# Optimization experiments

Measured on AMD Instinct MI355X. Metric: run time of the kernel, lower is better.

The kernel has to match this reference:

```python
import jax, jax.numpy as jnp
import numpy as np

EPS = 1e-5
NUM_HEADS = 8
BLOCK_SIZE = 8


def _ln(x, w, b):
    mu = jnp.mean(x, axis=-1, keepdims=True)
    var = jnp.mean((x - mu) ** 2, axis=-1, keepdims=True)
    return (x - mu) * jax.lax.rsqrt(var + EPS) * w + b


def _mha(x, wqkv, bqkv, wo, bo, allowed):
    # x: [b,t,d]; wqkv: [3d,d]; allowed: [t,t] bool (True = attend)
    b, t, d = x.shape
    h, hd = NUM_HEADS, d // NUM_HEADS
    qkv = x @ wqkv.T + bqkv
    q, k, v = jnp.split(qkv, 3, axis=-1)
    q = q.reshape(b, t, h, hd)
    k = k.reshape(b, t, h, hd)
    v = v.reshape(b, t, h, hd)
    scores = jnp.einsum('bihd,bjhd->bhij', q, k) / np.sqrt(hd).astype(x.dtype)
    scores = jnp.where(allowed[None, None], scores, -jnp.inf)
    attn = jax.nn.softmax(scores, axis=-1)
    out = jnp.einsum('bhij,bjhd->bihd', attn, v).reshape(b, t, d)
    return out @ wo.T + bo


def setup_inputs() -> dict:
    key = jax.random.key(0)
    ks = jax.random.split(key, 20)
    B, T, D, FF, L, MAXT = 64, 512, 256, 512, 4, 512
    s = 0.02
    return {
        'latents': jax.random.normal(ks[0], (B, T, D), dtype=jnp.float32),
        'move_ids': jax.random.randint(ks[1], (B, T), 0, 20480),
        'mask': jax.random.randint(ks[2], (B, T), 0, 2).astype(bool),
        'positional': s * jax.random.normal(ks[3], (1, MAXT, D), dtype=jnp.float32),
        'embed_from': s * jax.random.normal(ks[4], (64, D), dtype=jnp.float32),
        'embed_to': s * jax.random.normal(ks[5], (64, D), dtype=jnp.float32),
        'embed_promo': s * jax.random.normal(ks[6], (5, D), dtype=jnp.float32),
        'in_proj_w': s * jax.random.normal(ks[7], (L, 3 * D, D), dtype=jnp.float32),
        'in_proj_b': jnp.zeros((L, 3 * D), dtype=jnp.float32),
        'out_w': s * jax.random.normal(ks[8], (L, D, D), dtype=jnp.float32),
        'out_b': jnp.zeros((L, D), dtype=jnp.float32),
        'fc1_w': s * jax.random.normal(ks[9], (L, FF, D), dtype=jnp.float32),
        'fc1_b': jnp.zeros((L, FF), dtype=jnp.float32),
        'fc2_w': s * jax.random.normal(ks[10], (L, D, FF), dtype=jnp.float32),
        'fc2_b': jnp.zeros((L, D), dtype=jnp.float32),
        'norm_w': jnp.ones((D,), dtype=jnp.float32),
        'norm_b': jnp.zeros((D,), dtype=jnp.float32),
    }


def reference(latents, move_ids, mask, positional, embed_from, embed_to,
              embed_promo, in_proj_w, in_proj_b, out_w, out_b,
              fc1_w, fc1_b, fc2_w, fc2_b, norm_w, norm_b):
    b, t, d = latents.shape
    # move-id decomposition: promo/from/to embedding sum
    promo = move_ids // 4096
    rem = move_ids % 4096
    frm = rem // 64
    to = rem % 64
    x = latents + positional[:, :t, :] + embed_from[frm] + embed_to[to] + embed_promo[promo]
    # block-causal mask: token i may attend j iff block(j) <= block(i)
    bidx = jnp.arange(t) // BLOCK_SIZE
    allowed = bidx[None, :] <= bidx[:, None]
    n_layers = in_proj_w.shape[0]
    for l in range(n_layers):
        # NOTE: the single LayerNorm (norm_w, norm_b) is shared everywhere,
        # exactly as in the original module.
        x = x + _mha(_ln(x, norm_w, norm_b), in_proj_w[l], in_proj_b[l],
                     out_w[l], out_b[l], allowed)
        h1 = jax.nn.relu(_ln(x, norm_w, norm_b) @ fc1_w[l].T + fc1_b[l])
        x = x + h1 @ fc2_w[l].T + fc2_b[l]
    x = _ln(x, norm_w, norm_b)
    return jnp.where(mask[..., None], x, latents)
```

## Files before the change

### kernel.cpp

```cpp
#include <hip/hip_runtime.h>
#include <math.h>

#define Bv  64
#define Tv  512
#define Dv  256
#define FFv 512
#define Lv  4
#define BTv (Bv*Tv)
#define EPSv 1e-5f
#define QSC 0.25509402f

typedef __attribute__((ext_vector_type(8))) short short8;
typedef __attribute__((ext_vector_type(4))) float f32x4;
typedef unsigned short us;

#if __has_builtin(__builtin_amdgcn_exp2f)
#define EXP2(x) __builtin_amdgcn_exp2f(x)
#else
#define EXP2(x) exp2f(x)
#endif

__device__ __forceinline__ us f2bf(float f) {
    unsigned r;
    asm("v_cvt_pk_bf16_f32 %0, %1, 0" : "=v"(r) : "v"(f));
    return (us)r;
}
__device__ __forceinline__ unsigned pk2(float a, float b) {
    unsigned r;
    asm("v_cvt_pk_bf16_f32 %0, %1, %2" : "=v"(r) : "v"(a), "v"(b));
    return r;
}
__device__ __forceinline__ float wave_sum(float v) {
#pragma unroll
    for (int o = 32; o > 0; o >>= 1) v += __shfl_xor(v, o);
    return v;
}

__global__ __launch_bounds__(256) void cvtall_kernel(
    const float* __restrict__ qw, const float* __restrict__ ow,
    const float* __restrict__ f1, const float* __restrict__ f2,
    const float* __restrict__ qb,
    us* __restrict__ wq, us* __restrict__ wo, us* __restrict__ w1,
    us* __restrict__ w2, float* __restrict__ sb)
{
    int blk = blockIdx.x, tid = threadIdx.x;
    if (blk < 2048) {
        const float* s; us* d; int i; float sc = 1.0f;
        if (blk < 768)       { i = blk*256 + tid;        s = qw; d = wq;
                               sc = (((i >> 6) % 768) < 256) ? QSC : 1.0f; }
        else if (blk < 1024) { i = (blk-768)*256 + tid;  s = ow; d = wo; }
        else if (blk < 1536) { i = (blk-1024)*256 + tid; s = f1; d = w1; }
        else                 { i = (blk-1536)*256 + tid; s = f2; d = w2; }
        float4 v = ((const float4*)s)[i];
        uint2 o;
        o.x = pk2(v.x*sc, v.y*sc);
        o.y = pk2(v.z*sc, v.w*sc);
        ((uint2*)d)[i] = o;
    } else {
        int i = (blk-2048)*256 + tid;
        sb[i] = qb[i] * (((i % 768) < 256) ? QSC : 1.0f);
    }
}

__global__ __launch_bounds__(256) void embed_ln_kernel(
    const float* __restrict__ lat, const int* __restrict__ mids,
    const float* __restrict__ pos, const float* __restrict__ ef,
    const float* __restrict__ et,  const float* __restrict__ ep,
    const float* __restrict__ nw,  const float* __restrict__ nb,
    float* __restrict__ x, us* __restrict__ xn)
{
    int wv = threadIdx.x >> 6, lane = threadIdx.x & 63;
    size_t row = (size_t)blockIdx.x * 4 + wv;
    int t  = (int)(row & (Tv - 1));
    int id = mids[row];
    int promo = id >> 12;
    int rem   = id & 4095;
    int frm   = rem >> 6;
    int to    = rem & 63;
    float4 v  = ((const float4*)(lat + row*Dv))[lane];
    float4 pv = ((const float4*)(pos + (size_t)t*Dv))[lane];
    float4 fv = ((const float4*)(ef + (size_t)frm*Dv))[lane];
    float4 tv = ((const float4*)(et + (size_t)to*Dv))[lane];
    float4 ev = ((const float4*)(ep + (size_t)promo*Dv))[lane];
    v.x += pv.x + fv.x + tv.x + ev.x;
    v.y += pv.y + fv.y + tv.y + ev.y;
    v.z += pv.z + fv.z + tv.z + ev.z;
    v.w += pv.w + fv.w + tv.w + ev.w;
    ((float4*)(x + row*Dv))[lane] = v;
    float mu = wave_sum(v.x + v.y + v.z + v.w) * (1.0f/Dv);
    float dx = v.x-mu, dy = v.y-mu, dz = v.z-mu, dw = v.w-mu;
    float var = wave_sum(dx*dx + dy*dy + dz*dz + dw*dw) * (1.0f/Dv);
    float inv = rsqrtf(var + EPSv);
    float4 w4 = ((const float4*)nw)[lane];
    float4 b4 = ((const float4*)nb)[lane];
    uint2 o;
    o.x = pk2(dx*inv*w4.x + b4.x, dy*inv*w4.y + b4.y);
    o.y = pk2(dz*inv*w4.z + b4.z, dw*inv*w4.w + b4.w);
    ((uint2*)(xn + row*Dv))[lane] = o;
}

__global__ __launch_bounds__(256) void final_kernel(
    const float* __restrict__ x, const float* __restrict__ lat,
    const int* __restrict__ mask, const float* __restrict__ w,
    const float* __restrict__ b, float* __restrict__ out)
{
    int wv = threadIdx.x >> 6, lane = threadIdx.x & 63;
    size_t row = (size_t)blockIdx.x * 4 + wv;
    float4 v = ((const float4*)(x + row*Dv))[lane];
    float mu = wave_sum(v.x + v.y + v.z + v.w) * (1.0f/Dv);
    float dx = v.x-mu, dy = v.y-mu, dz = v.z-mu, dw = v.w-mu;
    float var = wave_sum(dx*dx + dy*dy + dz*dz + dw*dw) * (1.0f/Dv);
    float inv = rsqrtf(var + EPSv);
    float4 w4 = ((const float4*)w)[lane];
    float4 b4 = ((const float4*)b)[lane];
    float4 o;
    o.x = dx*inv*w4.x + b4.x;
    o.y = dy*inv*w4.y + b4.y;
    o.z = dz*inv*w4.z + b4.z;
    o.w = dw*inv*w4.w + b4.w;
    if (!mask[row]) o = ((const float4*)(lat + row*Dv))[lane];
    ((float4*)(out + row*Dv))[lane] = o;
}

template<int RELU>
__global__ __launch_bounds__(512, 2) void mm256sq_kernel(
    const us* __restrict__ A, const us* __restrict__ B,
    const float* __restrict__ bias, us* __restrict__ C,
    int M, int N, int K)
{
    __shared__ us As[2][256*64];
    __shared__ us Bs[2][256*64];
    int tid  = threadIdx.x;
    int lane = tid & 63;
    int wu   = __builtin_amdgcn_readfirstlane(tid >> 6);
    int m0 = blockIdx.x * 256, n0 = blockIdx.y * 256;
    int wm = wu & 1, wn = wu >> 1;
    f32x4 acc[8][4] = {};
    int srow = lane >> 3;
    int sg   = (lane & 7) ^ srow;
    const us* Ag = A + (size_t)m0 * K + sg*8;
    const us* Bg = B + (size_t)n0 * K + sg*8;
    int cc = lane & 15, q4 = lane >> 4;

#define STG(kk, bb) { \
    _Pragma("unroll") \
    for (int p = 0; p < 4; p++) { \
        int row = wu*32 + p*8; \
        __builtin_amdgcn_global_load_lds( \
            (const __attribute__((address_space(1))) unsigned int*)(Ag + (size_t)(row + srow)*K + (kk)), \
            (__attribute__((address_space(3))) unsigned int*)(&As[bb][row*64]), \
            16, 0, 0); \
        __builtin_amdgcn_global_load_lds( \
            (const __attribute__((address_space(1))) unsigned int*)(Bg + (size_t)(row + srow)*K + (kk)), \
            (__attribute__((address_space(3))) unsigned int*)(&Bs[bb][row*64]), \
            16, 0, 0); \
    } }

    STG(0, 0);
    __syncthreads();
    int nk = K >> 6;
    int cur = 0;
    for (int t = 0; t < nk; t++) {
        if (t + 1 < nk) {
            if (cur) STG((t+1)*64, 0) else STG((t+1)*64, 1)
        }
#pragma unroll
        for (int h = 0; h < 2; h++) {
            int pg = ((h*4 + q4) ^ (cc & 7)) * 8;
            short8 av[8], bv[4];
#pragma unroll
            for (int i = 0; i < 8; i++)
                av[i] = *(const short8*)(&As[cur][(wm*128 + i*16 + cc)*64 + pg]);
#pragma unroll
            for (int j = 0; j < 4; j++)
                bv[j] = *(const short8*)(&Bs[cur][(wn*64 + j*16 + cc)*64 + pg]);
#pragma unroll
            for (int i = 0; i < 8; i++)
#pragma unroll
                for (int j = 0; j < 4; j++)
                    acc[i][j] = __builtin_amdgcn_mfma_f32_16x16x32_bf16(av[i], bv[j], acc[i][j], 0, 0, 0);
        }
        __syncthreads();
        cur ^= 1;
    }
#undef STG
#pragma unroll
    for (int j = 0; j < 4; j++) {
        int n = n0 + wn*64 + j*16 + cc;
        float bj = bias[n];
#pragma unroll
        for (int i = 0; i < 8; i++) {
#pragma unroll
            for (int r = 0; r < 4; r++) {
                int m = m0 + wm*128 + i*16 + q4*4 + r;
                float v = acc[i][j][r] + bj;
                if (RELU) v = fmaxf(v, 0.f);
                C[(size_t)m * N + n] = f2bf(v);
            }
        }
    }
}

__global__ __launch_bounds__(256) void mm256_kernel(
    const us* __restrict__ A, const us* __restrict__ B,
    const float* __restrict__ bias, float* __restrict__ x,
    us* __restrict__ xn, const float* __restrict__ nw,
    const float* __restrict__ nb, int M, int K)
{
    __shared__ us As[64*64];
    __shared__ us Bs[256*64];
    __shared__ float red[64][4][2];
    __shared__ float mus[64], rss[64];
    int tid  = threadIdx.x;
    int lane = tid & 63;
    int wu   = __builtin_amdgcn_readfirstlane(tid >> 6);
    int m0 = blockIdx.x * 64;
    f32x4 acc[4][4] = {};
    int srow = lane >> 3;
    int sg   = (lane & 7) ^ srow;
    const us* Ag = A + (size_t)m0 * K + sg*8;
    const us* Bg = B + sg*8;
    int cc = lane & 15, q4 = lane >> 4;
    for (int k0 = 0; k0 < K; k0 += 64) {
        __syncthreads();
#pragma unroll
        for (int p = 0; p < 2; p++) {
            int row = wu*16 + p*8;
            __builtin_amdgcn_global_load_lds(
                (const __attribute__((address_space(1))) unsigned int*)(Ag + (size_t)(row + srow)*K + k0),
                (__attribute__((address_space(3))) unsigned int*)(As + row*64),
                16, 0, 0);
        }
#pragma unroll
        for (int p = 0; p < 8; p++) {
            int row = wu*64 + p*8;
            __builtin_amdgcn_global_load_lds(
                (const __attribute__((address_space(1))) unsigned int*)(Bg + (size_t)(row + srow)*K + k0),
                (__attribute__((address_space(3))) unsigned int*)(Bs + row*64),
                16, 0, 0);
        }
        __syncthreads();
#pragma unroll
        for (int h = 0; h < 2; h++) {
            int pg = ((h*4 + q4) ^ (cc & 7)) * 8;
            short8 av[4], bv[4];
#pragma unroll
            for (int i = 0; i < 4; i++)
                av[i] = *(const short8*)(As + (i*16 + cc)*64 + pg);
#pragma unroll
            for (int j = 0; j < 4; j++)
                bv[j] = *(const short8*)(Bs + (wu*64 + j*16 + cc)*64 + pg);
#pragma unroll
            for (int i = 0; i < 4; i++)
#pragma unroll
                for (int j = 0; j < 4; j++)
                    acc[i][j] = __builtin_amdgcn_mfma_f32_16x16x32_bf16(av[i], bv[j], acc[i][j], 0, 0, 0);
        }
    }
    float bb[4], nwv[4], nbv[4];
#pragma unroll
    for (int j = 0; j < 4; j++) {
        int n = wu*64 + j*16 + cc;
        bb[j] = bias[n]; nwv[j] = nw[n]; nbv[j] = nb[n];
    }
#pragma unroll
    for (int i = 0; i < 4; i++) {
        float s[4] = {0.f,0.f,0.f,0.f}, sq[4] = {0.f,0.f,0.f,0.f};
#pragma unroll
        for (int j = 0; j < 4; j++) {
#pragma unroll
            for (int r = 0; r < 4; r++) {
                int m = m0 + i*16 + q4*4 + r;
                size_t off = (size_t)m * Dv + wu*64 + j*16 + cc;
                float v = acc[i][j][r] + bb[j] + x[off];
                acc[i][j][r] = v;
                x[off] = v;
                s[r] += v; sq[r] += v*v;
            }
        }
#pragma unroll
        for (int r = 0; r < 4; r++) {
#pragma unroll
            for (int o = 1; o < 16; o <<= 1) {
                s[r]  += __shfl_xor(s[r],  o);
                sq[r] += __shfl_xor(sq[r], o);
            }
        }
        if (cc == 0) {
#pragma unroll
            for (int r = 0; r < 4; r++) {
                red[i*16 + q4*4 + r][wu][0] = s[r];
                red[i*16 + q4*4 + r][wu][1] = sq[r];
            }
        }
    }
    __syncthreads();
    if (tid < 64) {
        float ts = red[tid][0][0] + red[tid][1][0] + red[tid][2][0] + red[tid][3][0];
        float tq = red[tid][0][1] + red[tid][1][1] + red[tid][2][1] + red[tid][3][1];
        float mu = ts * (1.0f/Dv);
        float var = tq * (1.0f/Dv) - mu*mu;
        mus[tid] = mu;
        rss[tid] = rsqrtf(var + EPSv);
    }
    __syncthreads();
#pragma unroll
    for (int i = 0; i < 4; i++) {
#pragma unroll
        for (int r = 0; r < 4; r++) {
            int ml = i*16 + q4*4 + r;
            float mu = mus[ml], rv = rss[ml];
#pragma unroll
            for (int j = 0; j < 4; j++) {
                size_t off = (size_t)(m0 + ml) * Dv + wu*64 + j*16 + cc;
                xn[off] = f2bf((acc[i][j][r] - mu)*rv*nwv[j] + nbv[j]);
            }
        }
    }
}

__global__ __launch_bounds__(256) void attn_kernel(
    const us* __restrict__ qkv, us* __restrict__ ao)
{
    int blk = blockIdx.x;
    int b  = blk & 63;
    int h  = (blk >> 6) & 7;
    int qt = blk >> 9;
    int i0 = qt << 6;
    int tid = threadIdx.x;
    int lane = tid & 63;
    int wu = tid >> 6;

    __shared__ us Ks[2][64][40];
    __shared__ us Vt[2][32][72];
    __shared__ us Ps[4][16][72];
    __shared__ float Ls[4][16];

    size_t rowbase = (size_t)b * Tv;
    int c = lane & 15, q4 = lane >> 4;

    short8 qfrag = *(const short8*)(qkv + (rowbase + i0 + wu*16 + c)*768 + h*32 + q4*8);

    int skey = tid >> 2, sdc = (tid & 3) << 3;
    int vkey = tid & 63, vg = tid >> 6;
    const us* kgp = qkv + (rowbase + skey)*768 + 256 + h*32 + sdc;
    const us* vgp = qkv + (rowbase + vkey)*768 + 512 + h*32 + vg*8;

    f32x4 oacc[2] = {};
    float lsum = 0.f;
    int ntiles = qt + 1;

    short8 kreg = *(const short8*)(kgp);
    short8 vreg = *(const short8*)(vgp);
    *(short8*)&Ks[0][skey][sdc] = kreg;
#pragma unroll
    for (int j = 0; j < 8; j++) Vt[0][vg*8 + j][vkey] = vreg[j];
    if (ntiles > 1) {
        kreg = *(const short8*)(kgp + 64*768);
        vreg = *(const short8*)(vgp + 64*768);
    }
    __syncthreads();

    for (int kt = 0; kt < ntiles; kt++) {
        int cur = kt & 1;
        if (kt + 1 < ntiles) {
            *(short8*)&Ks[cur^1][skey][sdc] = kreg;
#pragma unroll
            for (int j = 0; j < 8; j++) Vt[cur^1][vg*8 + j][vkey] = vreg[j];
        }
        if (kt + 2 < ntiles) {
            kreg = *(const short8*)(kgp + (size_t)(kt+2)*64*768);
            vreg = *(const short8*)(vgp + (size_t)(kt+2)*64*768);
        }

        f32x4 st[4];
#pragma unroll
        for (int jt = 0; jt < 4; jt++) {
            short8 kf = *(const short8*)&Ks[cur][jt*16 + c][q4*8];
            st[jt] = __builtin_amdgcn_mfma_f32_16x16x32_bf16(kf, qfrag, (f32x4){0.f,0.f,0.f,0.f}, 0, 0, 0);
        }
        bool diag = (kt == ntiles - 1);
#pragma unroll
        for (int jt = 0; jt < 4; jt++) {
            float msk = (!diag || (2*jt + (q4 >> 1) <= 2*wu + (c >> 3))) ? 1.f : 0.f;
            float p0 = EXP2(st[jt][0]) * msk;
            float p1 = EXP2(st[jt][1]) * msk;
            float p2 = EXP2(st[jt][2]) * msk;
            float p3 = EXP2(st[jt][3]) * msk;
            lsum += p0 + p1 + p2 + p3;
            uint2 w2; w2.x = pk2(p0, p1); w2.y = pk2(p2, p3);
            *(uint2*)&Ps[wu][c][jt*16 + q4*4] = w2;
        }
#pragma unroll
        for (int kk = 0; kk < 2; kk++) {
            short8 pf = *(const short8*)&Ps[wu][c][kk*32 + q4*8];
#pragma unroll
            for (int dt = 0; dt < 2; dt++) {
                short8 vf = *(const short8*)&Vt[cur][dt*16 + c][kk*32 + q4*8];
                oacc[dt] = __builtin_amdgcn_mfma_f32_16x16x32_bf16(pf, vf, oacc[dt], 0, 0, 0);
            }
        }
        __syncthreads();
    }

    float l = lsum;
    l += __shfl_xor(l, 16);
    l += __shfl_xor(l, 32);
    if (q4 == 0) Ls[wu][c] = 1.0f / l;
    float4 lv4 = *(const float4*)&Ls[wu][q4*4];
#pragma unroll
    for (int dt = 0; dt < 2; dt++) {
#pragma unroll
        for (int r = 0; r < 4; r++) {
            float li = (r == 0) ? lv4.x : (r == 1) ? lv4.y : (r == 2) ? lv4.z : lv4.w;
            ao[(rowbase + i0 + wu*16 + q4*4 + r)*256 + h*32 + dt*16 + c] = f2bf(oacc[dt][r] * li);
        }
    }
}

extern "C" void kernel_launch(void* const* d_in, const int* in_sizes, int n_in,
                              void* d_out, int out_size, void* d_ws, size_t ws_size,
                              hipStream_t stream)
{
    const float* latents    = (const float*)d_in[0];
    const int*   move_ids   = (const int*)  d_in[1];
    const int*   mask       = (const int*)  d_in[2];
    const float* positional = (const float*)d_in[3];
    const float* embed_from = (const float*)d_in[4];
    const float* embed_to   = (const float*)d_in[5];
    const float* embed_promo= (const float*)d_in[6];
    const float* in_proj_w  = (const float*)d_in[7];
    const float* in_proj_b  = (const float*)d_in[8];
    const float* out_w      = (const float*)d_in[9];
    const float* out_b      = (const float*)d_in[10];
    const float* fc1_w      = (const float*)d_in[11];
    const float* fc1_b      = (const float*)d_in[12];
    const float* fc2_w      = (const float*)d_in[13];
    const float* fc2_b      = (const float*)d_in[14];
    const float* norm_w     = (const float*)d_in[15];
    const float* norm_b     = (const float*)d_in[16];
    float* out = (float*)d_out;

    float* x   = (float*)d_ws;
    float* sb  = x + (size_t)BTv * Dv;
    us* xn  = (us*)(sb + Lv*768);
    us* qkv = xn + (size_t)BTv * Dv;
    us* ao  = qkv + (size_t)BTv * 768;
    us* h1  = ao + (size_t)BTv * Dv;
    us* wq  = h1 + (size_t)BTv * FFv;
    us* wo  = wq + (size_t)Lv * 768 * Dv;
    us* w1  = wo + (size_t)Lv * Dv * Dv;
    us* w2  = w1 + (size_t)Lv * FFv * Dv;

    cvtall_kernel<<<2060, 256, 0, stream>>>(in_proj_w, out_w, fc1_w, fc2_w,
                                            in_proj_b, wq, wo, w1, w2, sb);

    embed_ln_kernel<<<BTv/4, 256, 0, stream>>>(latents, move_ids, positional,
        embed_from, embed_to, embed_promo, norm_w, norm_b, x, xn);

    for (int l = 0; l < Lv; l++) {
        mm256sq_kernel<0><<<dim3(BTv/256, 768/256), 512, 0, stream>>>(
            xn, wq + (size_t)l*768*Dv, sb + l*768, qkv, BTv, 768, Dv);
        attn_kernel<<<Bv*8*(Tv/64), 256, 0, stream>>>(qkv, ao);
        mm256_kernel<<<BTv/64, 256, 0, stream>>>(
            ao, wo + (size_t)l*Dv*Dv, out_b + l*Dv, x, xn, norm_w, norm_b,
            BTv, Dv);
        mm256sq_kernel<1><<<dim3(BTv/256, FFv/256), 512, 0, stream>>>(
            xn, w1 + (size_t)l*FFv*Dv, fc1_b + l*FFv, h1, BTv, FFv, Dv);
        mm256_kernel<<<BTv/64, 256, 0, stream>>>(
            h1, w2 + (size_t)l*Dv*FFv, fc2_b + l*Dv, x, xn, norm_w, norm_b,
            BTv, FFv);
    }
    final_kernel<<<BTv/4, 256, 0, stream>>>(x, latents, mask, norm_w, norm_b, out);
}
```

Baseline: 638.0 us.

## Retile GEMMs: 128x128 single-buffer projections, 128-row double-buffered fused residual-LN GEMM

The QKV and FC1 GEMMs move from 256x256 double-buffered tiles with 512 threads to 128x128 single-buffered tiles with 256 threads. That gives more blocks and lower LDS use per block, at the cost of less data reuse per tile. The fused residual+LayerNorm GEMM moves from 64-row tiles with 4 waves to 128-row tiles with 8 waves (a 2x4 wave grid) and double-buffered LDS staging, with cross-wave row reductions. The aim is better occupancy and load balance for the projections, and better B-matrix reuse plus load/compute overlap for the fused kernel.

```diff
diff --git a/kernel.cpp b/kernel.cpp
--- a/kernel.cpp
+++ b/kernel.cpp
@@ -123,33 +123,107 @@
 }
 
 template<int RELU>
-__global__ __launch_bounds__(512, 2) void mm256sq_kernel(
+__global__ __launch_bounds__(256) void mm_kernel(
     const us* __restrict__ A, const us* __restrict__ B,
     const float* __restrict__ bias, us* __restrict__ C,
     int M, int N, int K)
 {
-    __shared__ us As[2][256*64];
-    __shared__ us Bs[2][256*64];
+    __shared__ us As[128*64];
+    __shared__ us Bs[128*64];
     int tid  = threadIdx.x;
     int lane = tid & 63;
     int wu   = __builtin_amdgcn_readfirstlane(tid >> 6);
-    int m0 = blockIdx.x * 256, n0 = blockIdx.y * 256;
+    int m0 = blockIdx.x * 128, n0 = blockIdx.y * 128;
     int wm = wu & 1, wn = wu >> 1;
-    f32x4 acc[8][4] = {};
+    f32x4 acc[4][4] = {};
     int srow = lane >> 3;
     int sg   = (lane & 7) ^ srow;
     const us* Ag = A + (size_t)m0 * K + sg*8;
     const us* Bg = B + (size_t)n0 * K + sg*8;
     int cc = lane & 15, q4 = lane >> 4;
+    for (int k0 = 0; k0 < K; k0 += 64) {
+        __syncthreads();
+#pragma unroll
+        for (int p = 0; p < 4; p++) {
+            int row = wu*32 + p*8;
+            __builtin_amdgcn_global_load_lds(
+                (const __attribute__((address_space(1))) unsigned int*)(Ag + (size_t)(row + srow)*K + k0),
+                (__attribute__((address_space(3))) unsigned int*)(As + row*64),
+                16, 0, 0);
+            __builtin_amdgcn_global_load_lds(
+                (const __attribute__((address_space(1))) unsigned int*)(Bg + (size_t)(row + srow)*K + k0),
+                (__attribute__((address_space(3))) unsigned int*)(Bs + row*64),
+                16, 0, 0);
+        }
+        __syncthreads();
+#pragma unroll
+        for (int h = 0; h < 2; h++) {
+            int pg = ((h*4 + q4) ^ (cc & 7)) * 8;
+            short8 av[4], bv[4];
+#pragma unroll
+            for (int i = 0; i < 4; i++)
+                av[i] = *(const short8*)(As + (wm*64 + i*16 + cc)*64 + pg);
+#pragma unroll
+            for (int j = 0; j < 4; j++)
+                bv[j] = *(const short8*)(Bs + (wn*64 + j*16 + cc)*64 + pg);
+#pragma unroll
+            for (int i = 0; i < 4; i++)
+#pragma unroll
+                for (int j = 0; j < 4; j++)
+                    acc[i][j] = __builtin_amdgcn_mfma_f32_16x16x32_bf16(av[i], bv[j], acc[i][j], 0, 0, 0);
+        }
+    }
+#pragma unroll
+    for (int j = 0; j < 4; j++) {
+        int n = n0 + wn*64 + j*16 + cc;
+        float bj = bias[n];
+#pragma unroll
+        for (int i = 0; i < 4; i++) {
+#pragma unroll
+            for (int r = 0; r < 4; r++) {
+                int m = m0 + wm*64 + i*16 + q4*4 + r;
+                float v = acc[i][j][r] + bj;
+                if (RELU) v = fmaxf(v, 0.f);
+                C[(size_t)m * N + n] = f2bf(v);
+            }
+        }
+    }
+}
+
+__global__ __launch_bounds__(512) void mmfuse_kernel(
+    const us* __restrict__ A, const us* __restrict__ B,
+    const float* __restrict__ bias, float* __restrict__ x,
+    us* __restrict__ xn, const float* __restrict__ nw,
+    const float* __restrict__ nb, int M, int K)
+{
+    __shared__ us As[2][128*64];
+    __shared__ us Bs[2][256*64];
+    __shared__ float red[128][4][2];
+    __shared__ float mus[128], rss[128];
+    int tid  = threadIdx.x;
+    int lane = tid & 63;
+    int wu   = __builtin_amdgcn_readfirstlane(tid >> 6);
+    int m0 = blockIdx.x * 128;
+    int wm = wu & 1, wn = wu >> 1;
+    f32x4 acc[4][4] = {};
+    int srow = lane >> 3;
+    int sg   = (lane & 7) ^ srow;
+    const us* Ag = A + (size_t)m0 * K + sg*8;
+    const us* Bg = B + sg*8;
+    int cc = lane & 15, q4 = lane >> 4;
 
 #define STG(kk, bb) { \
     _Pragma("unroll") \
-    for (int p = 0; p < 4; p++) { \
-        int row = wu*32 + p*8; \
+    for (int p = 0; p < 2; p++) { \
+        int row = wu*16 + p*8; \
         __builtin_amdgcn_global_load_lds( \
             (const __attribute__((address_space(1))) unsigned int*)(Ag + (size_t)(row + srow)*K + (kk)), \
             (__attribute__((address_space(3))) unsigned int*)(&As[bb][row*64]), \
             16, 0, 0); \
+    } \
+    _Pragma("unroll") \
+    for (int p = 0; p < 4; p++) { \
+        int row = wu*32 + p*8; \
         __builtin_amdgcn_global_load_lds( \
             (const __attribute__((address_space(1))) unsigned int*)(Bg + (size_t)(row + srow)*K + (kk)), \
             (__attribute__((address_space(3))) unsigned int*)(&Bs[bb][row*64]), \
@@ -167,15 +241,15 @@
 #pragma unroll
         for (int h = 0; h < 2; h++) {
             int pg = ((h*4 + q4) ^ (cc & 7)) * 8;
-            short8 av[8], bv[4];
-#pragma unroll
-            for (int i = 0; i < 8; i++)
-                av[i] = *(const short8*)(&As[cur][(wm*128 + i*16 + cc)*64 + pg]);
+            short8 av[4], bv[4];
+#pragma unroll
+            for (int i = 0; i < 4; i++)
+                av[i] = *(const short8*)(&As[cur][(wm*64 + i*16 + cc)*64 + pg]);
 #pragma unroll
             for (int j = 0; j < 4; j++)
                 bv[j] = *(const short8*)(&Bs[cur][(wn*64 + j*16 + cc)*64 + pg]);
 #pragma unroll
-            for (int i = 0; i < 8; i++)
+            for (int i = 0; i < 4; i++)
 #pragma unroll
                 for (int j = 0; j < 4; j++)
                     acc[i][j] = __builtin_amdgcn_mfma_f32_16x16x32_bf16(av[i], bv[j], acc[i][j], 0, 0, 0);
@@ -184,84 +258,12 @@
         cur ^= 1;
     }
 #undef STG
+
+    float bb4[4], nwv[4], nbv[4];
 #pragma unroll
     for (int j = 0; j < 4; j++) {
-        int n = n0 + wn*64 + j*16 + cc;
-        float bj = bias[n];
-#pragma unroll
-        for (int i = 0; i < 8; i++) {
-#pragma unroll
-            for (int r = 0; r < 4; r++) {
-                int m = m0 + wm*128 + i*16 + q4*4 + r;
-                float v = acc[i][j][r] + bj;
-                if (RELU) v = fmaxf(v, 0.f);
-                C[(size_t)m * N + n] = f2bf(v);
-            }
-        }
-    }
-}
-
-__global__ __launch_bounds__(256) void mm256_kernel(
-    const us* __restrict__ A, const us* __restrict__ B,
-    const float* __restrict__ bias, float* __restrict__ x,
-    us* __restrict__ xn, const float* __restrict__ nw,
-    const float* __restrict__ nb, int M, int K)
-{
-    __shared__ us As[64*64];
-    __shared__ us Bs[256*64];
-    __shared__ float red[64][4][2];
-    __shared__ float mus[64], rss[64];
-    int tid  = threadIdx.x;
-    int lane = tid & 63;
-    int wu   = __builtin_amdgcn_readfirstlane(tid >> 6);
-    int m0 = blockIdx.x * 64;
-    f32x4 acc[4][4] = {};
-    int srow = lane >> 3;
-    int sg   = (lane & 7) ^ srow;
-    const us* Ag = A + (size_t)m0 * K + sg*8;
-    const us* Bg = B + sg*8;
-    int cc = lane & 15, q4 = lane >> 4;
-    for (int k0 = 0; k0 < K; k0 += 64) {
-        __syncthreads();
-#pragma unroll
-        for (int p = 0; p < 2; p++) {
-            int row = wu*16 + p*8;
-            __builtin_amdgcn_global_load_lds(
-                (const __attribute__((address_space(1))) unsigned int*)(Ag + (size_t)(row + srow)*K + k0),
-                (__attribute__((address_space(3))) unsigned int*)(As + row*64),
-                16, 0, 0);
-        }
-#pragma unroll
-        for (int p = 0; p < 8; p++) {
-            int row = wu*64 + p*8;
-            __builtin_amdgcn_global_load_lds(
-                (const __attribute__((address_space(1))) unsigned int*)(Bg + (size_t)(row + srow)*K + k0),
-                (__attribute__((address_space(3))) unsigned int*)(Bs + row*64),
-                16, 0, 0);
-        }
-        __syncthreads();
-#pragma unroll
-        for (int h = 0; h < 2; h++) {
-            int pg = ((h*4 + q4) ^ (cc & 7)) * 8;
-            short8 av[4], bv[4];
-#pragma unroll
-            for (int i = 0; i < 4; i++)
-                av[i] = *(const short8*)(As + (i*16 + cc)*64 + pg);
-#pragma unroll
-            for (int j = 0; j < 4; j++)
-                bv[j] = *(const short8*)(Bs + (wu*64 + j*16 + cc)*64 + pg);
-#pragma unroll
-            for (int i = 0; i < 4; i++)
-#pragma unroll
-                for (int j = 0; j < 4; j++)
-                    acc[i][j] = __builtin_amdgcn_mfma_f32_16x16x32_bf16(av[i], bv[j], acc[i][j], 0, 0, 0);
-        }
-    }
-    float bb[4], nwv[4], nbv[4];
-#pragma unroll
-    for (int j = 0; j < 4; j++) {
-        int n = wu*64 + j*16 + cc;
-        bb[j] = bias[n]; nwv[j] = nw[n]; nbv[j] = nb[n];
+        int n = wn*64 + j*16 + cc;
+        bb4[j] = bias[n]; nwv[j] = nw[n]; nbv[j] = nb[n];
     }
 #pragma unroll
     for (int i = 0; i < 4; i++) {
@@ -270,9 +272,9 @@
         for (int j = 0; j < 4; j++) {
 #pragma unroll
             for (int r = 0; r < 4; r++) {
-                int m = m0 + i*16 + q4*4 + r;
-                size_t off = (size_t)m * Dv + wu*64 + j*16 + cc;
-                float v = acc[i][j][r] + bb[j] + x[off];
+                int ml = wm*64 + i*16 + q4*4 + r;
+                size_t off = (size_t)(m0 + ml) * Dv + wn*64 + j*16 + cc;
+                float v = acc[i][j][r] + bb4[j] + x[off];
                 acc[i][j][r] = v;
                 x[off] = v;
                 s[r] += v; sq[r] += v*v;
@@ -289,13 +291,13 @@
         if (cc == 0) {
 #pragma unroll
             for (int r = 0; r < 4; r++) {
-                red[i*16 + q4*4 + r][wu][0] = s[r];
-                red[i*16 + q4*4 + r][wu][1] = sq[r];
+                red[wm*64 + i*16 + q4*4 + r][wn][0] = s[r];
+                red[wm*64 + i*16 + q4*4 + r][wn][1] = sq[r];
             }
         }
     }
     __syncthreads();
-    if (tid < 64) {
+    if (tid < 128) {
         float ts = red[tid][0][0] + red[tid][1][0] + red[tid][2][0] + red[tid][3][0];
         float tq = red[tid][0][1] + red[tid][1][1] + red[tid][2][1] + red[tid][3][1];
         float mu = ts * (1.0f/Dv);
@@ -308,11 +310,11 @@
     for (int i = 0; i < 4; i++) {
 #pragma unroll
         for (int r = 0; r < 4; r++) {
-            int ml = i*16 + q4*4 + r;
+            int ml = wm*64 + i*16 + q4*4 + r;
             float mu = mus[ml], rv = rss[ml];
 #pragma unroll
             for (int j = 0; j < 4; j++) {
-                size_t off = (size_t)(m0 + ml) * Dv + wu*64 + j*16 + cc;
+                size_t off = (size_t)(m0 + ml) * Dv + wn*64 + j*16 + cc;
                 xn[off] = f2bf((acc[i][j][r] - mu)*rv*nwv[j] + nbv[j]);
             }
         }
@@ -459,15 +461,15 @@
         embed_from, embed_to, embed_promo, norm_w, norm_b, x, xn);
 
     for (int l = 0; l < Lv; l++) {
-        mm256sq_kernel<0><<<dim3(BTv/256, 768/256), 512, 0, stream>>>(
+        mm_kernel<0><<<dim3(BTv/128, 768/128), 256, 0, stream>>>(
             xn, wq + (size_t)l*768*Dv, sb + l*768, qkv, BTv, 768, Dv);
         attn_kernel<<<Bv*8*(Tv/64), 256, 0, stream>>>(qkv, ao);
-        mm256_kernel<<<BTv/64, 256, 0, stream>>>(
+        mmfuse_kernel<<<BTv/128, 512, 0, stream>>>(
             ao, wo + (size_t)l*Dv*Dv, out_b + l*Dv, x, xn, norm_w, norm_b,
             BTv, Dv);
-        mm256sq_kernel<1><<<dim3(BTv/256, FFv/256), 512, 0, stream>>>(
+        mm_kernel<1><<<dim3(BTv/128, FFv/128), 256, 0, stream>>>(
             xn, w1 + (size_t)l*FFv*Dv, fc1_b + l*FFv, h1, BTv, FFv, Dv);
-        mm256_kernel<<<BTv/64, 256, 0, stream>>>(
+        mmfuse_kernel<<<BTv/128, 512, 0, stream>>>(
             h1, w2 + (size_t)l*Dv*FFv, fc2_b + l*Dv, x, xn, norm_w, norm_b,
             BTv, FFv);
     }
```

Measured after the change: 626.4 us. About the same (-1.8%).
